# Kernel optimization log

Hardware: AMD Instinct MI355X
Metric: run time of the kernel (lower is better)

The kernel has to match this reference:

```python
import jax, jax.numpy as jnp
import numpy as np

BATCH = 8
NDATA = 8192
NPOINT = 1024
NSAMPLE = 32
RADIUS = 0.2
CFEAT = 64


def setup_inputs() -> dict:
    key = jax.random.key(0)
    k1, k2, k3 = jax.random.split(key, 3)
    new_xyz = jax.random.normal(k1, (BATCH, NPOINT, 3), dtype=jnp.float32)
    xyz = jax.random.normal(k2, (BATCH, NDATA, 3), dtype=jnp.float32)
    points = jax.random.normal(k3, (BATCH, NDATA, CFEAT), dtype=jnp.float32)
    return {"new_xyz": new_xyz, "xyz": xyz, "points": points}


def reference(new_xyz, xyz, points):
    # Pairwise distances from every centroid to every dataset point.
    # delta: [B, P, N, 3]
    delta = xyz[:, None, :, :] - new_xyz[:, :, None, :]
    dist = jnp.linalg.norm(delta, axis=-1)  # [B, P, N]

    # Sort by distance (the original does a full argsort per centroid).
    sorted_idx = jnp.argsort(dist, axis=-1).astype(jnp.int32)  # [B, P, N]
    sorted_d = jnp.take_along_axis(dist, sorted_idx, axis=-1)  # [B, P, N]

    # Nearest point index replaces out-of-radius slots.
    nearest = sorted_idx[:, :, 0:1]  # [B, P, 1]
    radius_idx = jnp.where(sorted_d < RADIUS, sorted_idx, nearest)
    idx = radius_idx[:, :, :NSAMPLE]  # [B, P, S] int32 (ndataset >= nsample)

    # Batched gathers: grouped_xyz [B, P, S, 3], grouped_points [B, P, S, C].
    grouped_xyz = jnp.take_along_axis(
        xyz[:, None, :, :], idx[..., None], axis=2)
    grouped_points = jnp.take_along_axis(
        points[:, None, :, :], idx[..., None], axis=2)
    new_points = jnp.concatenate([grouped_xyz, grouped_points], axis=-1)
    return (new_points, idx, grouped_xyz)
```

## Files before the change

kernel.cpp:

```cpp
#include <hip/hip_runtime.h>
#include <math.h>

typedef unsigned int   u32;
typedef unsigned long long u64;

#define BATCH   8
#define NDATA   8192
#define NPOINT  1024
#define NSAMPLE 32
#define CFEAT   64
#define ROWF    67
#define MAXCAND 128
#define QPB     4
#define NB      256

#define OUT_IDX (BATCH*NPOINT*NSAMPLE*ROWF)
#define OUT_GX  (OUT_IDX + BATCH*NPOINT*NSAMPLE)

__device__ __forceinline__ float rnbf(float f) {
    u32 b = __float_as_uint(f);
    b += 0x7FFFu + ((b >> 16) & 1u);
    return __uint_as_float(b & 0xFFFF0000u);
}
__device__ __forceinline__ int clampidx(int v) {
    return (v < 0) ? 0 : (v > NDATA-1 ? NDATA-1 : v);
}
__device__ __forceinline__ int xbucket(float v) {
    int c = (int)floorf((v + 4.5f) * 28.444445f);
    return c < 0 ? 0 : (c > NB-1 ? NB-1 : c);
}

__global__ __launch_bounds__(1024)
void bin_kernel(const float* __restrict__ xyz,
                float4* __restrict__ wp, u32* __restrict__ wst)
{
    __shared__ u32 cnt[NB];
    __shared__ u32 sc[NB];
    const int b = blockIdx.x, tid = threadIdx.x;
    const float* bx = xyz + (size_t)b * NDATA * 3;

    if (tid < NB) cnt[tid] = 0;
    __syncthreads();
    for (int p = tid; p < NDATA; p += 1024)
        atomicAdd(&cnt[xbucket(bx[p*3])], 1u);
    __syncthreads();

    if (tid < NB) sc[tid] = cnt[tid];
    __syncthreads();
    #pragma unroll
    for (int d = 1; d < NB; d <<= 1) {
        u32 t = 0;
        if (tid < NB && tid >= d) t = sc[tid - d];
        __syncthreads();
        if (tid < NB && tid >= d) sc[tid] += t;
        __syncthreads();
    }
    if (tid < NB) {
        u32 excl = (tid == 0) ? 0u : sc[tid - 1];
        cnt[tid] = excl;
        wst[b*(NB+1) + tid] = excl;
        if (tid == 0) wst[b*(NB+1) + NB] = NDATA;
    }
    __syncthreads();

    for (int p = tid; p < NDATA; p += 1024) {
        float x = bx[p*3], y = bx[p*3+1], z = bx[p*3+2];
        u32 pos = atomicAdd(&cnt[xbucket(x)], 1u);
        wp[(size_t)b*NDATA + pos] = make_float4(x, y, z, __uint_as_float((u32)p));
    }
}

__global__ __launch_bounds__(256, 8)
void grouping_kernel(const float* __restrict__ new_xyz,
                     const float* __restrict__ xyz,
                     const float* __restrict__ points,
                     const float4* __restrict__ wp, const u32* __restrict__ wst,
                     float* __restrict__ out, float T)
{
    __shared__ float cand_s[QPB][MAXCAND];
    __shared__ int   cand_i[QPB][MAXCAND];
    __shared__ int   sel[QPB][NSAMPLE];

    const int tid  = threadIdx.x;
    const int wv   = tid >> 6;
    const int lane = tid & 63;
    const int q    = blockIdx.x * QPB + wv;
    const int b    = q >> 10;

    if (lane < NSAMPLE) sel[wv][lane] = 0;

    const float qx = new_xyz[q*3 + 0];
    const float qy = new_xyz[q*3 + 1];
    const float qz = new_xyz[q*3 + 2];
    const float*  bx = xyz + (size_t)b * NDATA * 3;
    const float4* cp = wp  + (size_t)b * NDATA;

    const int blo = xbucket(__fsub_rn(qx, 0.2005f));
    const int bhi = xbucket(__fadd_rn(qx, 0.2005f));
    const u32 j0 = wst[b*(NB+1) + blo];
    const u32 j1 = wst[b*(NB+1) + bhi + 1];

    int n = 0;
    for (u32 jb = j0; jb < j1; jb += 64) {
        u32 j  = jb + lane;
        bool in = j < j1;
        u32 jj = in ? j : (j1 - 1);
        float4 v = cp[jj];
        float dx = __fsub_rn(v.x, qx);
        float dy = __fsub_rn(v.y, qy);
        float dz = __fsub_rn(v.z, qz);
        float d2 = __fadd_rn(__fadd_rn(__fmul_rn(dx,dx), __fmul_rn(dy,dy)),
                             __fmul_rn(dz,dz));
        bool cc = in && (d2 < T);
        u64 m = __ballot(cc);
        if (m) {
            if (cc) {
                int below = __builtin_amdgcn_mbcnt_hi((u32)(m >> 32),
                             __builtin_amdgcn_mbcnt_lo((u32)m, 0));
                int pos = n + below;
                if (pos < MAXCAND) {
                    cand_s[wv][pos] = __fsqrt_rn(d2);
                    cand_i[wv][pos] = (int)__float_as_uint(v.w);
                }
            }
            n += (int)__popcll(m);
        }
    }

    int mini = 0;
    if (n == 0) {
        float mind = 3.402823466e38f; int mi = 0;
        for (int k = 0; k < NDATA/64; ++k) {
            int i = (k << 6) + lane;
            float dx = __fsub_rn(bx[i*3+0], qx);
            float dy = __fsub_rn(bx[i*3+1], qy);
            float dz = __fsub_rn(bx[i*3+2], qz);
            float d2 = __fadd_rn(__fadd_rn(__fmul_rn(dx,dx), __fmul_rn(dy,dy)),
                                 __fmul_rn(dz,dz));
            if (d2 < mind) { mind = d2; mi = i; }
        }
        float ms = __fsqrt_rn(mind);
        for (int off = 32; off; off >>= 1) {
            float os = __shfl_xor(ms, off);
            int   oi = __shfl_xor(mi, off);
            if (os < ms || (os == ms && oi < mi)) { ms = os; mi = oi; }
        }
        mini = mi;
    }

    __syncthreads();

    const int nj = n > MAXCAND ? MAXCAND : n;
    for (int kk = lane; kk < nj; kk += 64) {
        float sk = cand_s[wv][kk];
        int   ik = cand_i[wv][kk];
        int r = 0;
        for (int mm = 0; mm < nj; ++mm) {
            float sm = cand_s[wv][mm];
            int   im = cand_i[wv][mm];
            r += (int)((sm < sk) | ((sm == sk) & (im < ik)));
        }
        if (r < NSAMPLE) sel[wv][r] = clampidx(ik);
    }
    __syncthreads();
    {
        const int nsel = nj < NSAMPLE ? nj : NSAMPLE;
        if (lane >= nsel && lane < NSAMPLE) {
            int pad = (nj > 0) ? sel[wv][0] : clampidx(mini);
            sel[wv][lane] = pad;
        }
    }
    __syncthreads();

    if (lane < NSAMPLE)
        out[OUT_IDX + (size_t)q*NSAMPLE + lane] = rnbf((float)sel[wv][lane]);

    for (int e = lane; e < NSAMPLE*3; e += 64) {
        int sR = e / 3, c2 = e - sR*3;
        int is = sel[wv][sR];
        out[OUT_GX + (size_t)q*(NSAMPLE*3) + e] = rnbf(bx[is*3 + c2]);
    }

    const float* prow = points + (size_t)b * NDATA * CFEAT;
    float* onp = out + (size_t)q * (NSAMPLE*ROWF);
    #pragma unroll 2
    for (int e = lane; e < NSAMPLE*ROWF; e += 64) {
        int sR = e / ROWF;
        int c2 = e - sR*ROWF;
        int is = sel[wv][sR];
        const float* ap = (c2 < 3) ? (bx + (size_t)is*3 + c2)
                                   : (prow + (size_t)is*CFEAT + (c2-3));
        onp[e] = rnbf(*ap);
    }
}

extern "C" void kernel_launch(void* const* d_in, const int* in_sizes, int n_in,
                              void* d_out, int out_size, void* d_ws, size_t ws_size,
                              hipStream_t stream) {
    union { u32 u; float f; } lo, hi, mid;
    lo.u = 0u; hi.f = 0.05f;
    while (hi.u - lo.u > 1u) {
        mid.u = lo.u + (hi.u - lo.u) / 2u;
        if (sqrtf(mid.f) >= 0.2f) hi.u = mid.u; else lo.u = mid.u;
    }
    float T = hi.f;

    float4* wp  = (float4*)d_ws;
    u32*    wst = (u32*)(wp + (size_t)BATCH*NDATA);

    const float* nxz = (const float*)d_in[0];
    const float* xyz = (const float*)d_in[1];
    const float* pts = (const float*)d_in[2];

    bin_kernel<<<BATCH, 1024, 0, stream>>>(xyz, wp, wst);
    grouping_kernel<<<(BATCH*NPOINT)/QPB, 256, 0, stream>>>(
        nxz, xyz, pts, wp, wst, (float*)d_out, T);
}
```

Baseline: 129.6 us.

## Switch spatial binning from 1D x-buckets to a 2D x-y grid

After: 129.8 us. About the same (+0.1%).

```diff
diff --git a/kernel.cpp b/kernel.cpp
--- a/kernel.cpp
+++ b/kernel.cpp
@@ -12,7 +12,9 @@
 #define ROWF    67
 #define MAXCAND 128
 #define QPB     4
-#define NB      256
+#define NBX     64
+#define NBY     64
+#define NBT     (NBX*NBY)
 
 #define OUT_IDX (BATCH*NPOINT*NSAMPLE*ROWF)
 #define OUT_GX  (OUT_IDX + BATCH*NPOINT*NSAMPLE)
@@ -25,47 +27,54 @@
 __device__ __forceinline__ int clampidx(int v) {
     return (v < 0) ? 0 : (v > NDATA-1 ? NDATA-1 : v);
 }
-__device__ __forceinline__ int xbucket(float v) {
-    int c = (int)floorf((v + 4.5f) * 28.444445f);
-    return c < 0 ? 0 : (c > NB-1 ? NB-1 : c);
+__device__ __forceinline__ int bkt1(float v) {
+    int c = (int)floorf((v + 4.5f) * 7.1111112f);
+    return c < 0 ? 0 : (c > 63 ? 63 : c);
 }
 
 __global__ __launch_bounds__(1024)
 void bin_kernel(const float* __restrict__ xyz,
                 float4* __restrict__ wp, u32* __restrict__ wst)
 {
-    __shared__ u32 cnt[NB];
-    __shared__ u32 sc[NB];
+    __shared__ u32 cnt[NBT];
+    __shared__ u32 sc[1024];
     const int b = blockIdx.x, tid = threadIdx.x;
     const float* bx = xyz + (size_t)b * NDATA * 3;
 
-    if (tid < NB) cnt[tid] = 0;
-    __syncthreads();
-    for (int p = tid; p < NDATA; p += 1024)
-        atomicAdd(&cnt[xbucket(bx[p*3])], 1u);
-    __syncthreads();
-
-    if (tid < NB) sc[tid] = cnt[tid];
-    __syncthreads();
+    for (int i = tid; i < NBT; i += 1024) cnt[i] = 0;
+    __syncthreads();
+    for (int p = tid; p < NDATA; p += 1024) {
+        int bb = bkt1(bx[p*3]) * NBY + bkt1(bx[p*3+1]);
+        atomicAdd(&cnt[bb], 1u);
+    }
+    __syncthreads();
+
+    u32 c4[4]; u32 local = 0;
     #pragma unroll
-    for (int d = 1; d < NB; d <<= 1) {
+    for (int k = 0; k < 4; ++k) { c4[k] = cnt[4*tid + k]; local += c4[k]; }
+    sc[tid] = local;
+    __syncthreads();
+    for (int d = 1; d < 1024; d <<= 1) {
         u32 t = 0;
-        if (tid < NB && tid >= d) t = sc[tid - d];
+        if (tid >= d) t = sc[tid - d];
         __syncthreads();
-        if (tid < NB && tid >= d) sc[tid] += t;
+        if (tid >= d) sc[tid] += t;
         __syncthreads();
     }
-    if (tid < NB) {
-        u32 excl = (tid == 0) ? 0u : sc[tid - 1];
-        cnt[tid] = excl;
-        wst[b*(NB+1) + tid] = excl;
-        if (tid == 0) wst[b*(NB+1) + NB] = NDATA;
-    }
+    u32 run = (tid == 0) ? 0u : sc[tid - 1];
+    #pragma unroll
+    for (int k = 0; k < 4; ++k) {
+        wst[(size_t)b*(NBT+1) + 4*tid + k] = run;
+        cnt[4*tid + k] = run;
+        run += c4[k];
+    }
+    if (tid == 0) wst[(size_t)b*(NBT+1) + NBT] = NDATA;
     __syncthreads();
 
     for (int p = tid; p < NDATA; p += 1024) {
         float x = bx[p*3], y = bx[p*3+1], z = bx[p*3+2];
-        u32 pos = atomicAdd(&cnt[xbucket(x)], 1u);
+        int bb = bkt1(x) * NBY + bkt1(y);
+        u32 pos = atomicAdd(&cnt[bb], 1u);
         wp[(size_t)b*NDATA + pos] = make_float4(x, y, z, __uint_as_float((u32)p));
     }
 }
@@ -94,36 +103,41 @@
     const float qz = new_xyz[q*3 + 2];
     const float*  bx = xyz + (size_t)b * NDATA * 3;
     const float4* cp = wp  + (size_t)b * NDATA;
-
-    const int blo = xbucket(__fsub_rn(qx, 0.2005f));
-    const int bhi = xbucket(__fadd_rn(qx, 0.2005f));
-    const u32 j0 = wst[b*(NB+1) + blo];
-    const u32 j1 = wst[b*(NB+1) + bhi + 1];
+    const u32*    st = wst + (size_t)b * (NBT+1);
+
+    const int bxlo = bkt1(__fsub_rn(qx, 0.2005f));
+    const int bxhi = bkt1(__fadd_rn(qx, 0.2005f));
+    const int bylo = bkt1(__fsub_rn(qy, 0.2005f));
+    const int byhi = bkt1(__fadd_rn(qy, 0.2005f));
 
     int n = 0;
-    for (u32 jb = j0; jb < j1; jb += 64) {
-        u32 j  = jb + lane;
-        bool in = j < j1;
-        u32 jj = in ? j : (j1 - 1);
-        float4 v = cp[jj];
-        float dx = __fsub_rn(v.x, qx);
-        float dy = __fsub_rn(v.y, qy);
-        float dz = __fsub_rn(v.z, qz);
-        float d2 = __fadd_rn(__fadd_rn(__fmul_rn(dx,dx), __fmul_rn(dy,dy)),
-                             __fmul_rn(dz,dz));
-        bool cc = in && (d2 < T);
-        u64 m = __ballot(cc);
-        if (m) {
-            if (cc) {
-                int below = __builtin_amdgcn_mbcnt_hi((u32)(m >> 32),
-                             __builtin_amdgcn_mbcnt_lo((u32)m, 0));
-                int pos = n + below;
-                if (pos < MAXCAND) {
-                    cand_s[wv][pos] = __fsqrt_rn(d2);
-                    cand_i[wv][pos] = (int)__float_as_uint(v.w);
+    for (int bxi = bxlo; bxi <= bxhi; ++bxi) {
+        const u32 j0 = st[bxi*NBY + bylo];
+        const u32 j1 = st[bxi*NBY + byhi + 1];
+        for (u32 jb = j0; jb < j1; jb += 64) {
+            u32 j  = jb + lane;
+            bool in = j < j1;
+            u32 jj = in ? j : (j1 - 1);
+            float4 v = cp[jj];
+            float dx = __fsub_rn(v.x, qx);
+            float dy = __fsub_rn(v.y, qy);
+            float dz = __fsub_rn(v.z, qz);
+            float d2 = __fadd_rn(__fadd_rn(__fmul_rn(dx,dx), __fmul_rn(dy,dy)),
+                                 __fmul_rn(dz,dz));
+            bool cc = in && (d2 < T);
+            u64 m = __ballot(cc);
+            if (m) {
+                if (cc) {
+                    int below = __builtin_amdgcn_mbcnt_hi((u32)(m >> 32),
+                                 __builtin_amdgcn_mbcnt_lo((u32)m, 0));
+                    int pos = n + below;
+                    if (pos < MAXCAND) {
+                        cand_s[wv][pos] = __fsqrt_rn(d2);
+                        cand_i[wv][pos] = (int)__float_as_uint(v.w);
+                    }
                 }
+                n += (int)__popcll(m);
             }
-            n += (int)__popcll(m);
         }
     }
 
```
